# Optimization experiments

Measured on AMD Instinct MI355X. Metric: run time of the kernel, lower is better.

## Reference

```python
import jax, jax.numpy as jnp
import numpy as np
from jax import lax

N_IMG = 2
LEVEL_HW = [(200, 200), (100, 100), (50, 50), (25, 25), (13, 13)]
STRIDES = [4, 8, 16, 32, 64]
SIZES = [32.0, 64.0, 128.0, 256.0, 512.0]
A = 3
LEVEL_SIZES = [A * h * w for h, w in LEVEL_HW]
R = sum(LEVEL_SIZES)  # 159882
PRE_NMS = 1000   # pre_nms_top_n['testing']
POST_NMS = 1000  # post_nms_top_n['testing']
NMS_THRESH = 0.7
SCORE_THRESH = 0.0
MIN_SIZE = 1e-3
IMG_H = IMG_W = 800.0
BBOX_XFORM_CLIP = float(np.log(1000.0 / 16.0))


def _make_anchors():
    ratios = np.array([0.5, 1.0, 2.0])
    h_r = np.sqrt(ratios)
    w_r = 1.0 / h_r
    out = []
    for (h, w), stride, size in zip(LEVEL_HW, STRIDES, SIZES):
        ws = size * w_r
        hs = size * h_r
        base = np.stack([-ws / 2, -hs / 2, ws / 2, hs / 2], 1)  # [A,4]
        sx = (np.arange(w) + 0.5) * stride
        sy = (np.arange(h) + 0.5) * stride
        yy, xx = np.meshgrid(sy, sx, indexing='ij')
        shifts = np.stack([xx.ravel(), yy.ravel(), xx.ravel(), yy.ravel()], 1)  # [H*W,4]
        out.append((shifts[:, None, :] + base[None, :, :]).reshape(-1, 4))
    return np.concatenate(out, 0).astype(np.float32)  # [R,4]


def setup_inputs() -> dict:
    key = jax.random.key(0)
    k1, k2 = jax.random.split(key)
    objectness = jax.random.normal(k1, (N_IMG, R), jnp.float32)
    deltas = jax.random.normal(k2, (N_IMG, R, 4), jnp.float32) * 0.2
    anchors = jnp.asarray(_make_anchors())
    return {"objectness": objectness, "deltas": deltas, "anchors": anchors}


def _decode(deltas, anchors):
    # BoxCoder.decode with weights (1,1,1,1)
    wa = anchors[:, 2] - anchors[:, 0]
    ha = anchors[:, 3] - anchors[:, 1]
    cxa = anchors[:, 0] + 0.5 * wa
    cya = anchors[:, 1] + 0.5 * ha
    dx, dy, dw, dh = deltas[..., 0], deltas[..., 1], deltas[..., 2], deltas[..., 3]
    dw = jnp.minimum(dw, BBOX_XFORM_CLIP)
    dh = jnp.minimum(dh, BBOX_XFORM_CLIP)
    cx = dx * wa + cxa
    cy = dy * ha + cya
    w = jnp.exp(dw) * wa
    h = jnp.exp(dh) * ha
    return jnp.stack([cx - 0.5 * w, cy - 0.5 * h, cx + 0.5 * w, cy + 0.5 * h], -1)


def _nms_single(boxes, scores, lvl, valid):
    # batched_nms via per-level coordinate offset trick
    offs = lvl.astype(boxes.dtype) * (max(IMG_H, IMG_W) + 1.0)
    ob = boxes + offs[:, None]
    s = jnp.where(valid, scores, -1.0)
    order = jnp.argsort(-s)
    b = ob[order]          # offset boxes, score-descending
    raw = boxes[order]     # original boxes
    v = valid[order]
    ss = s[order]
    area = (b[:, 2] - b[:, 0]) * (b[:, 3] - b[:, 1])
    lt = jnp.maximum(b[:, None, :2], b[None, :, :2])
    rb = jnp.minimum(b[:, None, 2:], b[None, :, 2:])
    wh = jnp.clip(rb - lt, 0.0)
    inter = wh[..., 0] * wh[..., 1]
    iou = inter / (area[:, None] + area[None, :] - inter + 1e-9)  # [K,K]
    K = b.shape[0]

    def body(keep, i):
        suppressed = jnp.any(keep & (iou[:, i] > NMS_THRESH))
        keep = keep.at[i].set(v[i] & ~suppressed)
        return keep, None

    keep, _ = lax.scan(body, jnp.zeros((K,), bool), jnp.arange(K))
    # compact kept boxes (score order preserved) into fixed POST_NMS slots
    pos = jnp.where(keep, jnp.minimum(jnp.cumsum(keep) - 1, POST_NMS), POST_NMS)
    out_b = jnp.zeros((POST_NMS + 1, 4), boxes.dtype).at[pos].set(raw)[:POST_NMS]
    out_s = jnp.full((POST_NMS + 1,), -1.0, boxes.dtype).at[pos].set(ss)[:POST_NMS]
    return out_b, out_s


def _forward(objectness, deltas, anchors):
    proposals = _decode(deltas, anchors)  # [N,R,4]
    # per-level topk (pre_nms_top_n)
    idxs = []
    off = 0
    for n in LEVEL_SIZES:
        k = min(PRE_NMS, n)
        _, ti = lax.top_k(objectness[:, off:off + n], k)
        idxs.append(ti + off)
        off += n
    top_idx = jnp.concatenate(idxs, 1)  # [N,K]
    obj = jnp.take_along_axis(objectness, top_idx, 1)
    boxes = jnp.take_along_axis(proposals, top_idx[..., None], 1)
    levels = jnp.concatenate([jnp.full((n,), i, jnp.int32) for i, n in enumerate(LEVEL_SIZES)])
    lvl = levels[top_idx]
    scores = jax.nn.sigmoid(obj)
    # clip_boxes_to_image
    x1 = jnp.clip(boxes[..., 0], 0.0, IMG_W)
    y1 = jnp.clip(boxes[..., 1], 0.0, IMG_H)
    x2 = jnp.clip(boxes[..., 2], 0.0, IMG_W)
    y2 = jnp.clip(boxes[..., 3], 0.0, IMG_H)
    boxes = jnp.stack([x1, y1, x2, y2], -1)
    # remove_small_boxes + score_thresh -> validity mask (fixed shapes)
    valid = (x2 - x1 >= MIN_SIZE) & (y2 - y1 >= MIN_SIZE) & (scores >= SCORE_THRESH)
    return jax.vmap(_nms_single)(boxes, scores, lvl, valid)


def reference(objectness, deltas, anchors):
    return _forward(objectness, deltas, anchors)
```

## Files before the change

kernel.cpp:

```cpp
#include <hip/hip_runtime.h>

typedef unsigned long long u64;
typedef unsigned int u32;

#define R_TOT 159882
#define POST 1000
#define IMG_SZ 800.0f
#define NMS_TH 0.7f
#define BBOX_CLIP 4.135166556742356f
#define LCAP 1024

__device__ __forceinline__ float fadd_(float a, float b){ return __fadd_rn(a,b); }
__device__ __forceinline__ float fsub_(float a, float b){ return __fsub_rn(a,b); }
__device__ __forceinline__ float fmul_(float a, float b){ return __fmul_rn(a,b); }

__device__ __forceinline__ int lvl_len(int l){ const int L[5]={120000,30000,7500,1875,507}; return L[l]; }
__device__ __forceinline__ int lvl_off(int l){ const int L[5]={0,120000,150000,157500,159375}; return L[l]; }
__device__ __forceinline__ int lvl_k(int l){ const int L[5]={1000,1000,1000,1000,507}; return L[l]; }

__device__ __forceinline__ u32 mono_(u32 u){ return (u & 0x80000000u) ? ~u : (u | 0x80000000u); }

__device__ __forceinline__ u64 readlane64(u64 v, int i){
  u32 lo = (u32)__builtin_amdgcn_readlane((int)(u32)v, i);
  u32 hi = (u32)__builtin_amdgcn_readlane((int)(u32)(v >> 32), i);
  return ((u64)hi << 32) | (u64)lo;
}

__global__ __launch_bounds__(256) void k_front(const float* __restrict__ obj,
                                               int* histS,
                                               u64* mainS, u64* tieS,
                                               int* cntS, int* cnt2S){
  int g = blockIdx.x, sl = blockIdx.y;
  int img = g/5, lvl = g%5;
  int n = lvl_len(lvl), s0 = lvl_off(lvl), k = lvl_k(lvl);
  int tid = threadIdx.x, lane = tid & 63, wid = tid >> 6;
  __shared__ __align__(16) int lh[4096];
  __shared__ int wsum[4];
  __shared__ int sh_bs, lc, lc2;
  for (int i = tid; i < 4096; i += 256) lh[i] = 0;
  __syncthreads();
  int lo = (int)((long long)n * sl / 16), hiS = (int)((long long)n * (sl+1) / 16);
  int ns = hiS - lo;
  int ks = k < ns ? k : ns;
  const float* p = obj + img*R_TOT + s0;
  #pragma unroll 4
  for (int e = lo + tid; e < hiS; e += 256){
    u32 mu = mono_(__float_as_uint(p[e]));
    atomicAdd(&lh[(~mu) >> 20], 1);
  }
  __syncthreads();
  {
    int* dst = histS + (g*16 + sl)*4096;
    for (int i = tid; i < 4096; i += 256) dst[i] = lh[i];
  }
  int h[16];
  #pragma unroll
  for (int j = 0; j < 16; j++) h[j] = lh[16*tid + j];
  int part = 0;
  #pragma unroll
  for (int j = 0; j < 16; j++) part += h[j];
  int x = part;
  for (int d = 1; d < 64; d <<= 1){ int y = __shfl_up(x, d); if (lane >= d) x += y; }
  if (lane == 63) wsum[wid] = x;
  if (tid == 0){ lc = 0; lc2 = 0; }
  __syncthreads();
  int add = 0;
  for (int w = 0; w < wid; w++) add += wsum[w];
  int incl = x + add, excl = incl - part;
  if (excl < ks && ks <= incl){
    int cum = excl;
    #pragma unroll
    for (int q = 0; q < 16; q++){
      if (cum + h[q] >= ks){ sh_bs = 16*tid + q; break; }
      cum += h[q];
    }
  }
  __syncthreads();
  int bs = sh_bs;
  u64* lmain = (u64*)lh;
  u64* ltie  = (u64*)lh + 1024;
  #pragma unroll 4
  for (int e = lo + tid; e < hiS; e += 256){
    u32 mu = mono_(__float_as_uint(p[e]));
    u64 key56 = (((u64)(~mu)) << 24) | (u32)(s0 + e);
    int bin = (int)(key56 >> 44);
    if (bin < bs){ int pos = atomicAdd(&lc, 1); lmain[pos] = key56; }
    else if (bin == bs){ int pos = atomicAdd(&lc2, 1); if (pos < 1024) ltie[pos] = key56; }
  }
  __syncthreads();
  int idx16 = g*16 + sl;
  if (tid == 0){ cntS[idx16] = lc; cnt2S[idx16] = lc2; }
  for (int i = tid; i < lc; i += 256) mainS[idx16*1024 + i] = lmain[i];
  int c2l = lc2 < 1024 ? lc2 : 1024;
  for (int i = tid; i < c2l; i += 256) tieS[idx16*1024 + i] = ltie[i];
}

__global__ __launch_bounds__(1024) void k_seldecode(const float* __restrict__ obj,
                                                    const float4* __restrict__ deltas,
                                                    const float4* __restrict__ anchors,
                                                    const int* __restrict__ histS,
                                                    const u64* __restrict__ mainS,
                                                    const u64* __restrict__ tieS,
                                                    const int* __restrict__ cntS,
                                                    const int* __restrict__ cnt2S,
                                                    float4* boxL, float* scoreL,
                                                    float4* nbox, u64* okeyN, int* ncnt){
  int g = blockIdx.x, img = g/5, lvl = g%5;
  int s0 = lvl_off(lvl), n = lvl_len(lvl), k = lvl_k(lvl);
  const float* p = obj + img*R_TOT + s0;
  __shared__ u64 Lbuf[LCAP];
  __shared__ u64 mainL[1024];
  __shared__ __align__(16) float4 lbox[1024];
  __shared__ u64 lokey[1024];
  __shared__ unsigned char lval[1024];
  __shared__ int h16[16];
  __shared__ int scnt[16], tcnt[16];
  __shared__ int wsum16[16];
  __shared__ int sh_bs, sh_rem, sh_mc, sh_tc, sh_sc, sh_rem2, sh_ovf;
  __shared__ u64 sh_thr;
  int tid = threadIdx.x, lane = tid & 63, wid = tid >> 6;
  if (tid < 16){ scnt[tid] = cntS[g*16 + tid]; tcnt[tid] = cnt2S[g*16 + tid]; }
  mainL[tid] = ~0ull;
  __syncthreads();
  if (tid == 0){
    int o = 0;
    #pragma unroll
    for (int q = 0; q < 16; q++) if (tcnt[q] > 1024) o = 1;
    sh_ovf = o; sh_mc = 0; sh_tc = 0; sh_sc = 0;
  }
  int h0 = 0, h1 = 0, h2 = 0, h3 = 0;
  {
    const int* hb = histS + g*16*4096 + 4*tid;
    #pragma unroll
    for (int s2 = 0; s2 < 16; s2++){
      int4 a = *(const int4*)(hb + s2*4096);
      h0 += a.x; h1 += a.y; h2 += a.z; h3 += a.w;
    }
  }
  int part = h0 + h1 + h2 + h3;
  int x = part;
  for (int d = 1; d < 64; d <<= 1){ int y = __shfl_up(x, d); if (lane >= d) x += y; }
  if (lane == 63) wsum16[wid] = x;
  __syncthreads();
  int add = 0;
  for (int w = 0; w < wid; w++) add += wsum16[w];
  int incl = x + add, excl = incl - part;
  if (excl < k && k <= incl){
    int cum = excl;
    if (cum + h0 >= k){ sh_bs = 4*tid;   sh_rem = k - cum; }
    else { cum += h0;
      if (cum + h1 >= k){ sh_bs = 4*tid+1; sh_rem = k - cum; }
      else { cum += h1;
        if (cum + h2 >= k){ sh_bs = 4*tid+2; sh_rem = k - cum; }
        else { cum += h2;    sh_bs = 4*tid+3; sh_rem = k - cum; }
      }
    }
  }
  __syncthreads();
  int bs = sh_bs;
  if (!sh_ovf){
    int mc = scnt[wid];
    int tcc = tcnt[wid] < 1024 ? tcnt[wid] : 1024;
    const u64* msrc = mainS + ((size_t)(g*16 + wid))*1024;
    const u64* tsrc = tieS + ((size_t)(g*16 + wid))*1024;
    for (int base = 0; base < mc; base += 256){
      int i0 = base + lane;
      u64 v0 = msrc[(i0       < mc) ? i0       : 0];
      u64 v1 = msrc[(i0+64    < mc) ? i0+64    : 0];
      u64 v2 = msrc[(i0+128   < mc) ? i0+128   : 0];
      u64 v3 = msrc[(i0+192   < mc) ? i0+192   : 0];
      #define PUSH(cond, vv) if (cond){ int b_ = (int)((vv) >> 44); \
        if (b_ < bs){ int pos = atomicAdd(&sh_mc, 1); mainL[pos] = (vv); } \
        else if (b_ == bs){ int pos = atomicAdd(&sh_tc, 1); if (pos < LCAP) Lbuf[pos] = (vv); } }
      PUSH(i0 < mc, v0) PUSH(i0+64 < mc, v1) PUSH(i0+128 < mc, v2) PUSH(i0+192 < mc, v3)
    }
    for (int base = 0; base < tcc; base += 256){
      int i0 = base + lane;
      u64 v0 = tsrc[(i0       < tcc) ? i0       : 0];
      u64 v1 = tsrc[(i0+64    < tcc) ? i0+64    : 0];
      u64 v2 = tsrc[(i0+128   < tcc) ? i0+128   : 0];
      u64 v3 = tsrc[(i0+192   < tcc) ? i0+192   : 0];
      PUSH(i0 < tcc, v0) PUSH(i0+64 < tcc, v1) PUSH(i0+128 < tcc, v2) PUSH(i0+192 < tcc, v3)
      #undef PUSH
    }
    __syncthreads();
    int nb = sh_mc, c2r = sh_tc, rem = sh_rem;
    if (c2r <= LCAP){
      for (int e = tid; e < c2r; e += 1024){
        u64 kk = Lbuf[e];
        int rk = 0;
        for (int qq = 0; qq < c2r; qq++) rk += (Lbuf[qq] < kk) ? 1 : 0;
        if (rk < rem){ int p2 = atomicAdd(&sh_sc, 1); mainL[nb + p2] = kk; }
      }
    } else {
      if (tid == 0) sh_ovf = 1;
    }
    __syncthreads();
  }
  if (sh_ovf){
    int* fh = (int*)lbox;
    for (int i = tid; i < 4096; i += 1024) fh[i] = 0;
    if (tid == 0){ sh_mc = 0; sh_sc = 0; }
    __syncthreads();
    for (int e = tid; e < n; e += 1024){
      u32 mu = mono_(__float_as_uint(p[e]));
      atomicAdd(&fh[(int)((~mu) >> 20)], 1);
    }
    __syncthreads();
    int f0 = fh[4*tid], f1 = fh[4*tid+1], f2 = fh[4*tid+2], f3 = fh[4*tid+3];
    int fpart = f0 + f1 + f2 + f3;
    int fx = fpart;
    for (int d = 1; d < 64; d <<= 1){ int y = __shfl_up(fx, d); if (lane >= d) fx += y; }
    if (lane == 63) wsum16[wid] = fx;
    __syncthreads();
    int fadd2 = 0;
    for (int w = 0; w < wid; w++) fadd2 += wsum16[w];
    int fincl = fx + fadd2, fexcl = fincl - fpart;
    if (fexcl < k && k <= fincl){
      int cum = fexcl;
      if (cum + f0 >= k){ sh_bs = 4*tid;   sh_rem = k - cum; }
      else { cum += f0;
        if (cum + f1 >= k){ sh_bs = 4*tid+1; sh_rem = k - cum; }
        else { cum += f1;
          if (cum + f2 >= k){ sh_bs = 4*tid+2; sh_rem = k - cum; }
          else { cum += f2;    sh_bs = 4*tid+3; sh_rem = k - cum; }
        }
      }
    }
    mainL[tid] = ~0ull;
    __syncthreads();
    int fbs = sh_bs;
    for (int e = tid; e < n; e += 1024){
      u32 mu = mono_(__float_as_uint(p[e]));
      u64 kk = (((u64)(~mu)) << 24) | (u32)(s0 + e);
      if ((int)(kk >> 44) < fbs){ int pos = atomicAdd(&sh_mc, 1); mainL[pos] = kk; }
    }
    __syncthreads();
    int nb = sh_mc;
    if (tid == 0){ sh_thr = ((u64)fbs) << 44; sh_rem2 = sh_rem; }
    __syncthreads();
    for (int shift = 40; shift >= 0; shift -= 4){
      if (tid < 16) h16[tid] = 0;
      __syncthreads();
      u64 pref = sh_thr;
      u64 himask = ~((1ull << (shift+4)) - 1ull);
      for (int e = tid; e < n; e += 1024){
        u32 mu = mono_(__float_as_uint(p[e]));
        u64 kk = (((u64)(~mu)) << 24) | (u32)(s0 + e);
        if ((kk & himask) == (pref & himask)) atomicAdd(&h16[(int)((kk >> shift) & 15)], 1);
      }
      __syncthreads();
      if (tid == 0){
        int r2 = sh_rem2, cum = 0;
        for (int d = 0; d < 16; d++){
          int hb2 = h16[d];
          if (cum + hb2 >= r2){ sh_thr = pref | ((u64)d << shift); sh_rem2 = r2 - cum; break; }
          cum += hb2;
        }
      }
      __syncthreads();
    }
    u64 thr = sh_thr;
    for (int e = tid; e < n; e += 1024){
      u32 mu = mono_(__float_as_uint(p[e]));
      u64 kk = (((u64)(~mu)) << 24) | (u32)(s0 + e);
      if ((int)(kk >> 44) == fbs && kk <= thr){ int p2 = atomicAdd(&sh_sc, 1); mainL[nb + p2] = kk; }
    }
    __syncthreads();
  }
  for (int k2 = 2; k2 <= 1024; k2 <<= 1){
    for (int j = k2 >> 1; j > 0; j >>= 1){
      __syncthreads();
      int i = tid, ixj = i ^ j;
      if (ixj > i){
        u64 a = mainL[i], b = mainL[ixj];
        bool up = (i & k2) == 0;
        if ((a > b) == up){ mainL[i] = b; mainL[ixj] = a; }
      }
    }
  }
  __syncthreads();
  int r = tid, t = g*1024 + r;
  if (r < k){
    int idx = (int)(mainL[r] & 0xFFFFFFu);
    float4 a = anchors[idx];
    float4 d = deltas[img*R_TOT + idx];
    float o = obj[img*R_TOT + idx];
    float wa = fsub_(a.z, a.x), ha = fsub_(a.w, a.y);
    float cxa = fadd_(a.x, fmul_(0.5f, wa)), cya = fadd_(a.y, fmul_(0.5f, ha));
    float dw = fminf(d.z, BBOX_CLIP), dh = fminf(d.w, BBOX_CLIP);
    float cx = fadd_(fmul_(d.x, wa), cxa), cy = fadd_(fmul_(d.y, ha), cya);
    float w  = fmul_(expf(dw), wa),        h  = fmul_(expf(dh), ha);
    float x1 = fsub_(cx, fmul_(0.5f, w)), y1 = fsub_(cy, fmul_(0.5f, h));
    float x2 = fadd_(cx, fmul_(0.5f, w)), y2 = fadd_(cy, fmul_(0.5f, h));
    x1 = fminf(fmaxf(x1, 0.0f), IMG_SZ); y1 = fminf(fmaxf(y1, 0.0f), IMG_SZ);
    x2 = fminf(fmaxf(x2, 0.0f), IMG_SZ); y2 = fminf(fmaxf(y2, 0.0f), IMG_SZ);
    bool valid = (fsub_(x2, x1) >= 1e-3f) && (fsub_(y2, y1) >= 1e-3f);
    float e = expf(-o);
    float sig = __fdiv_rn(1.0f, fadd_(1.0f, e));
    float s = valid ? sig : -1.0f;
    u32 sb = __float_as_uint(s);
    u32 ms = (sb & 0x80000000u) ? ~sb : (sb | 0x80000000u);
    float4 b4 = make_float4(x1, y1, x2, y2);
    boxL[t] = b4;
    scoreL[t] = sig;
    lokey[r] = (((u64)(~ms)) << 32) | (u32)(lvl*1000 + r);
    lbox[r] = b4;
    lval[r] = valid ? 1 : 0;
  } else {
    lval[r] = 0;
  }
  __syncthreads();
  if (tid < 64){
    int cnt = 0;
    float off = (float)lvl * 801.0f;
    for (int base = 0; base < k; base += 64){
      int r2 = base + lane;
      bool v = (r2 < k) && lval[r2];
      float4 b = lbox[r2 < k ? r2 : 0];
      u64 mask = __ballot(v);
      int before = __popcll(mask & ((1ull << lane) - 1ull));
      if (v){
        int pos = cnt + before;
        nbox[g*1024 + pos] = make_float4(fadd_(b.x,off), fadd_(b.y,off), fadd_(b.z,off), fadd_(b.w,off));
        okeyN[g*1024 + pos] = lokey[r2];
      }
      cnt += __popcll(mask);
    }
    if (lane == 0) ncnt[g] = cnt;
  }
}

__global__ __launch_bounds__(64) void k_mask(const float4* __restrict__ nbox,
                                             const int* __restrict__ ncnt,
                                             u64* LTG2){
  int g = blockIdx.x, tr = blockIdx.y, tw = blockIdx.z;
  if (tw > tr) return;
  int m = ncnt[g];
  if (tr*64 >= m) return;
  __shared__ float4 shb[64];
  __shared__ float sharea[64];
  int lane = threadIdx.x;
  if (tw*64 + lane < m){
    float4 b = nbox[g*1024 + tw*64 + lane];
    shb[lane] = b;
    sharea[lane] = fmul_(fsub_(b.z,b.x), fsub_(b.w,b.y));
  }
  __syncthreads();
  int j = tr*64 + lane;
  if (j >= m) return;
  float4 a = nbox[g*1024 + j];
  float areaA = fmul_(fsub_(a.z,a.x), fsub_(a.w,a.y));
  int imax = m - tw*64; if (imax > 64) imax = 64;
  if (tw == tr){
    u64 bitsF = 0;
    for (int ii = lane+1; ii < imax; ii++){
      float4 b = shb[ii];
      float ltx = fmaxf(a.x, b.x), lty = fmaxf(a.y, b.y);
      float rbx = fminf(a.z, b.z), rby = fminf(a.w, b.w);
      float wx = fmaxf(fsub_(rbx, ltx), 0.0f), wy = fmaxf(fsub_(rby, lty), 0.0f);
      float inter = fmul_(wx, wy);
      float den = fadd_(fsub_(fadd_(areaA, sharea[ii]), inter), 1e-9f);
      if (__fdiv_rn(inter, den) > NMS_TH) bitsF |= (1ull << ii);
    }
    LTG2[((size_t)(g*1024 + j))*16 + 15] = bitsF;
  } else {
    u64 bits = 0;
    for (int ii = 0; ii < imax; ii++){
      float4 b = shb[ii];
      float ltx = fmaxf(a.x, b.x), lty = fmaxf(a.y, b.y);
      float rbx = fminf(a.z, b.z), rby = fminf(a.w, b.w);
      float wx = fmaxf(fsub_(rbx, ltx), 0.0f), wy = fmaxf(fsub_(rby, lty), 0.0f);
      float inter = fmul_(wx, wy);
      float den = fadd_(fsub_(fadd_(areaA, sharea[ii]), inter), 1e-9f);
      if (__fdiv_rn(inter, den) > NMS_TH) bits |= (1ull << ii);
    }
    LTG2[((size_t)(g*1024 + j))*16 + tw] = bits;
  }
}

struct ChunkBuf {
  ulonglong2 v0, v1, v2, v3, v4, v5, v6, v7;
  u64 ok;
};

__device__ __forceinline__ void issue_chunk(const u64* __restrict__ LT2,
                                            const u64* __restrict__ oK,
                                            int c, int lane, ChunkBuf& b){
  int row = c*64 + lane;
  const ulonglong2* rp = (const ulonglong2*)(LT2 + (size_t)row*16);
  b.v0 = rp[0]; b.v1 = rp[1]; b.v2 = rp[2]; b.v3 = rp[3];
  b.v4 = rp[4]; b.v5 = rp[5]; b.v6 = rp[6]; b.v7 = rp[7];
  b.ok = oK[row];
}

__device__ __forceinline__ void consume_chunk(const ChunkBuf& b, int c, int m, int lane,
                                              u64* KwR, u64* runsL, int& cnt){
  int row = c*64 + lane;
  bool inr = row < m;
  u64 supp = 0;
  #define TERM(q, val) supp |= (((q) < c) ? (val) : 0ull) & KwR[q];
  TERM(0,  b.v0.x) TERM(1,  b.v0.y) TERM(2,  b.v1.x) TERM(3,  b.v1.y)
  TERM(4,  b.v2.x) TERM(5,  b.v2.y) TERM(6,  b.v3.x) TERM(7,  b.v3.y)
  TERM(8,  b.v4.x) TERM(9,  b.v4.y) TERM(10, b.v5.x) TERM(11, b.v5.y)
  TERM(12, b.v6.x) TERM(13, b.v6.y) TERM(14, b.v7.x)
  #undef TERM
  u64 fwd = inr ? b.v7.y : 0;
  u64 live = __ballot(inr && (supp == 0));
  u64 fz = __ballot(fwd != 0);
  u64 kept = 0;
  while (1){
    u64 lf = live & fz;
    if (!lf){ kept |= live; break; }
    int i = __builtin_ctzll(lf);
    u64 bi = 1ull << i;
    u64 below = live & (bi - 1ull);
    kept |= below | bi;
    live &= ~(below | bi);
    live &= ~readlane64(fwd, i);
  }
  KwR[c] = kept;
  bool kp = (kept >> lane) & 1ull;
  int before = __popcll(kept & ((1ull << lane) - 1ull));
  if (kp) runsL[cnt + before] = b.ok;
  cnt += __popcll(kept);
}

__global__ __launch_bounds__(1024) void k_scanmerge(const u64* __restrict__ LTG2,
                                                    const int* __restrict__ ncnt,
                                                    const u64* __restrict__ okeyN,
                                                    const float4* __restrict__ boxL,
                                                    const float* __restrict__ scoreL,
                                                    float* out){
  int img = blockIdx.x, tid = threadIdx.x, lane = tid & 63, wid = tid >> 6;
  __shared__ u64 runs[5*1024];
  __shared__ u64 Kw[5][16];
  __shared__ int cl[5];
  if (wid < 5){
    int l = wid, g = img*5 + l;
    int m = ncnt[g];
    int nch = (m + 63) >> 6;
    const u64* LT2 = LTG2 + ((size_t)g*1024)*16;
    const u64* oK = okeyN + g*1024;
    u64* KwR = &Kw[l][0];
    u64* runsL = &runs[l*1024];
    int cnt = 0;
    ChunkBuf A, B;
    if (nch > 0){
      issue_chunk(LT2, oK, 0, lane, A);
      int c = 0;
      while (c < nch){
        if (c+1 < nch) issue_chunk(LT2, oK, c+1, lane, B);
        consume_chunk(A, c, m, lane, KwR, runsL, cnt);
        c++;
        if (c >= nch) break;
        if (c+1 < nch) issue_chunk(LT2, oK, c+1, lane, A);
        consume_chunk(B, c, m, lane, KwR, runsL, cnt);
        c++;
      }
    }
    if (lane == 0) cl[l] = cnt;
  } else {
    for (int t = tid - 320; t < POST; t += 704){
      out[img*POST*4 + t*4 + 0] = 0.0f;
      out[img*POST*4 + t*4 + 1] = 0.0f;
      out[img*POST*4 + t*4 + 2] = 0.0f;
      out[img*POST*4 + t*4 + 3] = 0.0f;
      out[2*POST*4 + img*POST + t] = -1.0f;
    }
  }
  __syncthreads();
  for (int idx = tid; idx < 5*1024; idx += 1024){
    int l = idx >> 10, i = idx & 1023;
    if (i < cl[l]){
      u64 key = runs[l*1024 + i];
      int o0 = l+1; if (o0 >= 5) o0 -= 5;
      int o1 = l+2; if (o1 >= 5) o1 -= 5;
      int o2 = l+3; if (o2 >= 5) o2 -= 5;
      int o3 = l+4; if (o3 >= 5) o3 -= 5;
      const u64* r0 = runs + (o0 << 10);
      const u64* r1 = runs + (o1 << 10);
      const u64* r2 = runs + (o2 << 10);
      const u64* r3 = runs + (o3 << 10);
      int lo0 = 0, hi0 = cl[o0];
      int lo1 = 0, hi1 = cl[o1];
      int lo2 = 0, hi2 = cl[o2];
      int lo3 = 0, hi3 = cl[o3];
      #pragma unroll 1
      for (int st = 0; st < 11; st++){
        int m0 = (lo0+hi0)>>1, m1 = (lo1+hi1)>>1, m2 = (lo2+hi2)>>1, m3 = (lo3+hi3)>>1;
        u64 a0 = r0[m0], a1 = r1[m1], a2 = r2[m2], a3 = r3[m3];
        if (lo0 < hi0){ if (a0 < key) lo0 = m0+1; else hi0 = m0; }
        if (lo1 < hi1){ if (a1 < key) lo1 = m1+1; else hi1 = m1; }
        if (lo2 < hi2){ if (a2 < key) lo2 = m2+1; else hi2 = m2; }
        if (lo3 < hi3){ if (a3 < key) lo3 = m3+1; else hi3 = m3; }
      }
      int rank = i + lo0 + lo1 + lo2 + lo3;
      if (rank < POST){
        int pos = (int)(key & 0xFFFFFFFFull);
        int lvl = pos / 1000, r = pos - lvl*1000;
        int gg = img*5 + lvl;
        float4 bo = boxL[gg*1024 + r];
        float sc = scoreL[gg*1024 + r];
        out[img*POST*4 + rank*4 + 0] = bo.x;
        out[img*POST*4 + rank*4 + 1] = bo.y;
        out[img*POST*4 + rank*4 + 2] = bo.z;
        out[img*POST*4 + rank*4 + 3] = bo.w;
        out[2*POST*4 + img*POST + rank] = sc;
      }
    }
  }
}

extern "C" void kernel_launch(void* const* d_in, const int* in_sizes, int n_in,
                              void* d_out, int out_size, void* d_ws, size_t ws_size,
                              hipStream_t stream){
  (void)in_sizes; (void)n_in; (void)out_size; (void)ws_size;
  const float*  obj     = (const float*)d_in[0];
  const float4* deltas  = (const float4*)d_in[1];
  const float4* anchors = (const float4*)d_in[2];
  float* out = (float*)d_out;
  char* ws = (char*)d_ws;
  int* histS   = (int*)(ws + 0);
  u64* mainS   = (u64*)(ws + 2621440);
  u64* tieS    = (u64*)(ws + 3932160);
  int* cntS    = (int*)(ws + 5242880);
  int* cnt2S   = (int*)(ws + 5243520);
  float4* boxL = (float4*)(ws + 5244160);
  float* scoreL= (float*)(ws + 5408000);
  u64* okeyN   = (u64*)(ws + 5448960);
  float4* nbox = (float4*)(ws + 5530880);
  u64* LTG2    = (u64*)(ws + 5694720);
  int* ncnt    = (int*)(ws + 7005440);

  {
    dim3 gf(10, 16);
    k_front<<<gf, 256, 0, stream>>>(obj, histS, mainS, tieS, cntS, cnt2S);
  }
  k_seldecode<<<10, 1024, 0, stream>>>(obj, deltas, anchors, histS, mainS, tieS, cntS, cnt2S,
                                       boxL, scoreL, nbox, okeyN, ncnt);
  {
    dim3 gm(10, 16, 16);
    k_mask<<<gm, 64, 0, stream>>>(nbox, ncnt, LTG2);
  }
  k_scanmerge<<<2, 1024, 0, stream>>>(LTG2, ncnt, okeyN, boxL, scoreL, out);
}
```

Measured before the change: 160.6 us.

## Refine tie-bucket selection with a second-level histogram and trim bitonic-sort barriers

The boundary-bucket candidates were previously ranked by an all-pairs comparison over up to 1024 keys. That step is replaced with a second 12-bit histogram pass: a block prefix scan finds the sub-bucket holding the cutoff, keys below it are emitted directly, and only the keys in that sub-bucket are ranked pairwise. Separately, the shared-memory bitonic sort now drops __syncthreads for stages whose partner stays inside the same 64-lane wave, using volatile LDS accesses and wave-synchronous execution. The trade-off is extra histogram and scan passes with more barriers in the selection step, plus reliance on wave64 lockstep semantics for correctness of the sort.

```diff
diff --git a/kernel.cpp b/kernel.cpp
--- a/kernel.cpp
+++ b/kernel.cpp
@@ -117,6 +117,7 @@
   __shared__ int scnt[16], tcnt[16];
   __shared__ int wsum16[16];
   __shared__ int sh_bs, sh_rem, sh_mc, sh_tc, sh_sc, sh_rem2, sh_ovf;
+  __shared__ int sh_bs2, sh_rem2b, sh_c3;
   __shared__ u64 sh_thr;
   int tid = threadIdx.x, lane = tid & 63, wid = tid >> 6;
   if (tid < 16){ scnt[tid] = cntS[g*16 + tid]; tcnt[tid] = cnt2S[g*16 + tid]; }
@@ -126,7 +127,7 @@
     int o = 0;
     #pragma unroll
     for (int q = 0; q < 16; q++) if (tcnt[q] > 1024) o = 1;
-    sh_ovf = o; sh_mc = 0; sh_tc = 0; sh_sc = 0;
+    sh_ovf = o; sh_mc = 0; sh_tc = 0; sh_sc = 0; sh_c3 = 0;
   }
   int h0 = 0, h1 = 0, h2 = 0, h3 = 0;
   {
@@ -186,11 +187,50 @@
     __syncthreads();
     int nb = sh_mc, c2r = sh_tc, rem = sh_rem;
     if (c2r <= LCAP){
+      int* chist = (int*)lbox;
+      for (int i = tid; i < 4096; i += 1024) chist[i] = 0;
+      __syncthreads();
       for (int e = tid; e < c2r; e += 1024){
         u64 kk = Lbuf[e];
+        atomicAdd(&chist[(int)((kk >> 32) & 0xFFFu)], 1);
+      }
+      __syncthreads();
+      int t0 = chist[4*tid], t1 = chist[4*tid+1], t2 = chist[4*tid+2], t3 = chist[4*tid+3];
+      int tpart = t0 + t1 + t2 + t3;
+      int tx = tpart;
+      for (int d = 1; d < 64; d <<= 1){ int y = __shfl_up(tx, d); if (lane >= d) tx += y; }
+      if (lane == 63) wsum16[wid] = tx;
+      __syncthreads();
+      int tadd = 0;
+      for (int w = 0; w < wid; w++) tadd += wsum16[w];
+      int tincl = tx + tadd, texcl = tincl - tpart;
+      if (texcl < rem && rem <= tincl){
+        int cum = texcl;
+        if (cum + t0 >= rem){ sh_bs2 = 4*tid;   sh_rem2b = rem - cum; }
+        else { cum += t0;
+          if (cum + t1 >= rem){ sh_bs2 = 4*tid+1; sh_rem2b = rem - cum; }
+          else { cum += t1;
+            if (cum + t2 >= rem){ sh_bs2 = 4*tid+2; sh_rem2b = rem - cum; }
+            else { cum += t2;    sh_bs2 = 4*tid+3; sh_rem2b = rem - cum; }
+          }
+        }
+      }
+      __syncthreads();
+      int bs2 = sh_bs2;
+      u64* subT = lokey;
+      for (int e = tid; e < c2r; e += 1024){
+        u64 kk = Lbuf[e];
+        int sb2 = (int)((kk >> 32) & 0xFFFu);
+        if (sb2 < bs2){ int p2 = atomicAdd(&sh_sc, 1); mainL[nb + p2] = kk; }
+        else if (sb2 == bs2){ int p3 = atomicAdd(&sh_c3, 1); subT[p3] = kk; }
+      }
+      __syncthreads();
+      int c3 = sh_c3, rem2b = sh_rem2b;
+      for (int e = tid; e < c3; e += 1024){
+        u64 kk = subT[e];
         int rk = 0;
-        for (int qq = 0; qq < c2r; qq++) rk += (Lbuf[qq] < kk) ? 1 : 0;
-        if (rk < rem){ int p2 = atomicAdd(&sh_sc, 1); mainL[nb + p2] = kk; }
+        for (int qq = 0; qq < c3; qq++) rk += (subT[qq] < kk) ? 1 : 0;
+        if (rk < rem2b){ int p2 = atomicAdd(&sh_sc, 1); mainL[nb + p2] = kk; }
       }
     } else {
       if (tid == 0) sh_ovf = 1;
@@ -268,14 +308,17 @@
     }
     __syncthreads();
   }
-  for (int k2 = 2; k2 <= 1024; k2 <<= 1){
-    for (int j = k2 >> 1; j > 0; j >>= 1){
-      __syncthreads();
-      int i = tid, ixj = i ^ j;
-      if (ixj > i){
-        u64 a = mainL[i], b = mainL[ixj];
-        bool up = (i & k2) == 0;
-        if ((a > b) == up){ mainL[i] = b; mainL[ixj] = a; }
+  {
+    volatile u64* vmain = mainL;
+    for (int k2 = 2; k2 <= 1024; k2 <<= 1){
+      for (int j = k2 >> 1; j > 0; j >>= 1){
+        if (j >= 64 || (j == 32 && k2 >= 128)) __syncthreads();
+        int i = tid, ixj = i ^ j;
+        if (ixj > i){
+          u64 a = vmain[i], b = vmain[ixj];
+          bool up = (i & k2) == 0;
+          if ((a > b) == up){ vmain[i] = b; vmain[ixj] = a; }
+        }
       }
     }
   }
```

Result: slower. 166.6 us (+3.7%).
